# Performance work log

Measured on AMD Instinct MI355X. Metric: run time of the kernel, lower is better.

Reference implementation:

```python
import jax, jax.numpy as jnp
import numpy as np

B, C, T, H, W = 32, 384, 16, 14, 14
K, NUM_SAMPLES, SIGMA = 8, 1000, 0.05
C2 = 2 * C  # ScoreNet doubles embed_dim internally


def setup_inputs() -> dict:
    key = jax.random.key(0)
    ks = jax.random.split(key, 12)
    def rn(k, shape, s=0.02):
        return jax.random.normal(k, shape, dtype=jnp.float32) * s
    return {
        "frames": jax.random.normal(ks[0], (B, C, T, H, W), dtype=jnp.float32),
        "noise": jax.random.normal(ks[1], (B, NUM_SAMPLES, T), dtype=jnp.float32),
        "conv_w": rn(ks[2], (C, C, 1, 3, 3)),
        "conv_b": jnp.zeros((C,), jnp.float32),
        "bn_g": jnp.ones((C,), jnp.float32),
        "bn_b": jnp.zeros((C,), jnp.float32),
        "ln_g": jnp.ones((C2,), jnp.float32),
        "ln_b": jnp.zeros((C2,), jnp.float32),
        "lin_w": rn(ks[3], (C2, C2)),
        "lin_b": jnp.zeros((C2,), jnp.float32),
        "w1": rn(ks[4], (C2, C)), "b1": jnp.zeros((C,), jnp.float32),
        "w2": rn(ks[5], (C, C // 2)), "b2": jnp.zeros((C // 2,), jnp.float32),
        "w3": rn(ks[6], (C // 2, 1)), "b3": jnp.zeros((1,), jnp.float32),
    }


def score_net(frames, conv_w, conv_b, bn_g, bn_b, ln_g, ln_b, lin_w, lin_b,
              w1, b1, w2, b2, w3, b3):
    x = jax.lax.stop_gradient(frames)  # ScoreNet detaches its input
    x = jax.lax.conv_general_dilated(
        x, conv_w, window_strides=(1, 2, 2), padding='VALID',
        dimension_numbers=('NCDHW', 'OIDHW', 'NCDHW'))
    x = x + conv_b[None, :, None, None, None]
    # BatchNorm3d in training mode: biased batch stats over (N,T,H,W)
    m = x.mean(axis=(0, 2, 3, 4))
    v = x.var(axis=(0, 2, 3, 4))
    x = (x - m[None, :, None, None, None]) / jnp.sqrt(v + 1e-5)[None, :, None, None, None]
    x = x * bn_g[None, :, None, None, None] + bn_b[None, :, None, None, None]
    # b c t h w -> b t (h w) c
    b, c, t, h, w = x.shape
    x = jnp.transpose(x, (0, 2, 3, 4, 1)).reshape(b, t, h * w, c)
    x = jnp.concatenate([x.mean(axis=2), x.max(axis=2)], axis=-1)  # [B,T,2C]
    # LayerNorm(2C)
    mu = x.mean(-1, keepdims=True)
    var = x.var(-1, keepdims=True)
    x = (x - mu) / jnp.sqrt(var + 1e-5) * ln_g + ln_b
    x = jax.nn.gelu(x @ lin_w + lin_b, approximate=False)
    local_x = x[..., :C2 // 2]
    global_x = jnp.broadcast_to(x[..., C2 // 2:].mean(axis=1, keepdims=True), (b, t, C2 // 2))
    x = jnp.concatenate([local_x, global_x], axis=-1)
    x = jax.nn.gelu(x @ w1 + b1, approximate=False)
    x = jax.nn.gelu(x @ w2 + b2, approximate=False)
    score = (x @ w3 + b3)[..., 0]  # [B,T]
    smin = score.min(axis=-1, keepdims=True)
    smax = score.max(axis=-1, keepdims=True)
    return (score - smin) / (smax - smin + 1e-5)


def perturbed_indicators(score, noise):
    d = score.shape[-1]
    pert = score[:, None, :] + noise * SIGMA  # [B,N,T]
    idx_top = jnp.sort(jax.lax.top_k(pert, K)[1], axis=-1)        # [B,N,K]
    idx_back = jnp.sort(jax.lax.top_k(-pert, d - K)[1], axis=-1)  # [B,N,T-K]
    ind_top = jax.nn.one_hot(idx_top, d, dtype=jnp.float32).mean(axis=1)   # [B,K,T]
    ind_back = jax.nn.one_hot(idx_back, d, dtype=jnp.float32).mean(axis=1)  # [B,T-K,T]
    return ind_top, ind_back


def reference(frames, noise, conv_w, conv_b, bn_g, bn_b, ln_g, ln_b, lin_w, lin_b,
              w1, b1, w2, b2, w3, b3):
    score = score_net(frames, conv_w, conv_b, bn_g, bn_b, ln_g, ln_b, lin_w, lin_b,
                      w1, b1, w2, b2, w3, b3)  # [B,T]
    ind_top, ind_back = perturbed_indicators(score, noise)
    # b c t h w -> b t (h w c)
    flat = jnp.transpose(frames, (0, 2, 3, 4, 1)).reshape(B, T, H * W * C)
    p_top = jnp.einsum('bkd,bdc->bkc', ind_top, flat)
    p_back = jnp.einsum('bkd,bdc->bkc', ind_back, flat)
    frames_topk = jnp.transpose(p_top.reshape(B, K, H, W, C), (0, 4, 1, 2, 3))
    frames_back = jnp.transpose(p_back.reshape(B, T - K, H, W, C), (0, 4, 1, 2, 3))
    sorted_inds = jnp.argsort(score, axis=1)
    return frames_topk, frames_back, sorted_inds
```

## Files before the change

kernel.cpp:

```cpp
#include <hip/hip_runtime.h>
#include <hip/hip_bf16.h>
#include <cstdint>

#define NB 32
#define NC 384
#define NT 16
#define NH 14
#define NW 14
#define HWI 196
#define HOW 6
#define HWO 36
#define C2 768
#define MCONV (NB*NT*HWO)
#define KCONV 3456
#define TOPK 8
#define NSAMP 1000
#define OUT_TOPK_ELEMS (NB*NC*TOPK*HWI)
#define OUT_INDS_OFF   (2*OUT_TOPK_ELEMS)

#define OFF_FHI  0ull
#define OFF_FLO  77070336ull
#define OFF_WHI  154140672ull
#define OFF_WLO  156794880ull
#define OFF_CONV 159449088ull
#define OFF_PART 0ull
#define OFF_BNSC 221184ull
#define OFF_BNSH 222720ull
#define OFF_Y    224256ull
#define OFF_X1   1797120ull
#define OFF_GM   3369984ull
#define OFF_X2   3419136ull
#define OFF_H1   4992000ull
#define OFF_H2   5778432ull
#define OFF_IND  6171648ull

typedef __attribute__((ext_vector_type(4))) float f32x4;
typedef __attribute__((ext_vector_type(8))) short bf16x8;

__device__ __forceinline__ unsigned short f2bf(float f) {
  unsigned u = __float_as_uint(f);
  unsigned r = (u + 0x7FFFu + ((u >> 16) & 1u)) >> 16;
  return (unsigned short)r;
}
__device__ __forceinline__ float bf2f(unsigned short u) {
  return __uint_as_float(((unsigned)u) << 16);
}

__device__ __forceinline__ void gload_lds16(const void* gptr, void* lptr) {
  __builtin_amdgcn_global_load_lds(
      (const __attribute__((address_space(1))) unsigned int*)gptr,
      (__attribute__((address_space(3))) unsigned int*)lptr, 16, 0, 0);
}

__global__ __launch_bounds__(256)
void split_frames(const float* __restrict__ fr,
                  unsigned short* __restrict__ fhi,
                  unsigned short* __restrict__ flo) {
  __shared__ float tile[64][50];
  int bid = blockIdx.x;
  int cb = bid % 6;
  int r  = bid / 6;
  int hwb = r % 4;
  int bt  = r / 4;
  int c0 = cb * 64, hw0 = hwb * 49;
  int b = bt >> 4, t = bt & 15;
  size_t base = (((size_t)b * NC + c0) * NT + t) * HWI + hw0;
  for (int idx = threadIdx.x; idx < 64 * 49; idx += 256) {
    int c = idx / 49, hw = idx % 49;
    tile[c][hw] = fr[base + (size_t)c * (NT * HWI) + hw];
  }
  __syncthreads();
  size_t obase = ((size_t)bt * HWI + hw0) * NC + c0;
  for (int idx = threadIdx.x; idx < 64 * 49; idx += 256) {
    int hw = idx >> 6, c = idx & 63;
    float v = tile[c][hw];
    unsigned short h = f2bf(v);
    unsigned short l = f2bf(v - bf2f(h));
    size_t o = obase + (size_t)hw * NC + c;
    fhi[o] = h; flo[o] = l;
  }
}

__global__ __launch_bounds__(256)
void split_w(const float* __restrict__ cw,
             unsigned short* __restrict__ whi,
             unsigned short* __restrict__ wlo) {
  int idx = blockIdx.x * 256 + threadIdx.x;
  int co = idx / KCONV;
  int rem = idx - co * KCONV;
  int c9 = rem / NC, ci = rem - c9 * NC;
  float v = cw[((size_t)co * NC + ci) * 9 + c9];
  unsigned short h = f2bf(v);
  unsigned short l = f2bf(v - bf2f(h));
  whi[idx] = h; wlo[idx] = l;
}

__global__ __launch_bounds__(256, 2)
void conv_gemm(const unsigned short* __restrict__ fhi,
               const unsigned short* __restrict__ flo,
               const unsigned short* __restrict__ whi,
               const unsigned short* __restrict__ wlo,
               const float* __restrict__ conv_b,
               float* __restrict__ out) {
  __shared__ unsigned short sAhi[128 * 32], sAlo[128 * 32];
  __shared__ unsigned short sBhi[128 * 32], sBlo[128 * 32];
  const int tid = threadIdx.x;
  const int lane = tid & 63;
  const int wv = tid >> 6;
  const int bid = blockIdx.x;
  const int bm = bid % 144;
  const int bn = bid / 144;

  int aoff[2], boff[2];
#pragma unroll
  for (int j = 0; j < 2; ++j) {
    int l = (wv * 2 + j) * 64 + lane;
    int row = l >> 2, chunk = l & 3;
    int m = bm * 128 + row;
    int wo = m % 6; int tmp = m / 6;
    int ho = tmp % 6; tmp /= 6;
    aoff[j] = ((tmp * HWI) + (2 * ho) * NW + 2 * wo) * NC + chunk * 8;
    int co = bn * 128 + row;
    boff[j] = co * KCONV + chunk * 8;
  }

  f32x4 acc[4][4];
#pragma unroll
  for (int i = 0; i < 4; ++i)
#pragma unroll
    for (int j = 0; j < 4; ++j) acc[i][j] = (f32x4){0.f, 0.f, 0.f, 0.f};

  const int wrow = (wv >> 1) * 64;
  const int wcol = (wv & 1) * 64;
  const int fr_row = lane & 15;
  const int fr_k = (lane >> 4) * 8;

  for (int step = 0; step < 108; ++step) {
    int c9 = step / 12;
    int cis = (step - c9 * 12) * 32;
    int kh = c9 / 3, kw = c9 - kh * 3;
    int soffA = (kh * NW + kw) * NC + cis;
    int soffB = c9 * NC + cis;
#pragma unroll
    for (int j = 0; j < 2; ++j) {
      char* ldsA = (char*)sAhi + (wv * 2 + j) * 1024;
      char* ldsAl = (char*)sAlo + (wv * 2 + j) * 1024;
      char* ldsB = (char*)sBhi + (wv * 2 + j) * 1024;
      char* ldsBl = (char*)sBlo + (wv * 2 + j) * 1024;
      gload_lds16(fhi + aoff[j] + soffA, ldsA);
      gload_lds16(flo + aoff[j] + soffA, ldsAl);
      gload_lds16(whi + boff[j] + soffB, ldsB);
      gload_lds16(wlo + boff[j] + soffB, ldsBl);
    }
    __syncthreads();
    bf16x8 ah[4], al[4], bh[4], bl[4];
#pragma unroll
    for (int m = 0; m < 4; ++m) {
      int r = wrow + m * 16 + fr_row;
      ah[m] = *(const bf16x8*)&sAhi[r * 32 + fr_k];
      al[m] = *(const bf16x8*)&sAlo[r * 32 + fr_k];
    }
#pragma unroll
    for (int n = 0; n < 4; ++n) {
      int r = wcol + n * 16 + fr_row;
      bh[n] = *(const bf16x8*)&sBhi[r * 32 + fr_k];
      bl[n] = *(const bf16x8*)&sBlo[r * 32 + fr_k];
    }
#pragma unroll
    for (int m = 0; m < 4; ++m)
#pragma unroll
      for (int n = 0; n < 4; ++n) {
        acc[m][n] = __builtin_amdgcn_mfma_f32_16x16x32_bf16(ah[m], bh[n], acc[m][n], 0, 0, 0);
        acc[m][n] = __builtin_amdgcn_mfma_f32_16x16x32_bf16(ah[m], bl[n], acc[m][n], 0, 0, 0);
        acc[m][n] = __builtin_amdgcn_mfma_f32_16x16x32_bf16(al[m], bh[n], acc[m][n], 0, 0, 0);
      }
    __syncthreads();
  }

#pragma unroll
  for (int m = 0; m < 4; ++m)
#pragma unroll
    for (int n = 0; n < 4; ++n) {
      int col = bn * 128 + wcol + n * 16 + (lane & 15);
      float cb = conv_b[col];
#pragma unroll
      for (int j = 0; j < 4; ++j) {
        int row = bm * 128 + wrow + m * 16 + (lane >> 4) * 4 + j;
        out[(size_t)row * NC + col] = acc[m][n][j] + cb;
      }
    }
}

__global__ __launch_bounds__(384)
void bn_part(const float* __restrict__ conv, float* __restrict__ part) {
  int c = threadIdx.x;
  int r0 = blockIdx.x * 256;
  float s = 0.f, sq = 0.f;
  for (int r = 0; r < 256; ++r) {
    float v = conv[(size_t)(r0 + r) * NC + c];
    s += v; sq += v * v;
  }
  part[blockIdx.x * 768 + c] = s;
  part[blockIdx.x * 768 + 384 + c] = sq;
}

__global__ __launch_bounds__(384)
void bn_fin(const float* __restrict__ part, const float* __restrict__ bn_g,
            const float* __restrict__ bn_b, float* __restrict__ bnsc,
            float* __restrict__ bnsh) {
  int c = threadIdx.x;
  float s = 0.f, sq = 0.f;
  for (int i = 0; i < 72; ++i) {
    s += part[i * 768 + c];
    sq += part[i * 768 + 384 + c];
  }
  float mean = s / (float)MCONV;
  float var = sq / (float)MCONV - mean * mean;
  float sc = bn_g[c] / sqrtf(var + 1e-5f);
  bnsc[c] = sc;
  bnsh[c] = bn_b[c] - mean * sc;
}

__global__ __launch_bounds__(384)
void pool_ln(const float* __restrict__ conv, const float* __restrict__ bnsc,
             const float* __restrict__ bnsh, const float* __restrict__ ln_g,
             const float* __restrict__ ln_b, float* __restrict__ y) {
  __shared__ float r1[384], r2[384], stats[2];
  int bt = blockIdx.x, c = threadIdx.x;
  float sc = bnsc[c], sh = bnsh[c];
  const float* p = conv + (size_t)bt * HWO * NC + c;
  float sum = 0.f, mx = -1e30f;
  for (int hw = 0; hw < HWO; ++hw) {
    float v = p[hw * NC] * sc + sh;
    sum += v;
    mx = fmaxf(mx, v);
  }
  float meanv = sum * (1.f / 36.f);
  r1[c] = meanv + mx;
  r2[c] = meanv * meanv + mx * mx;
  __syncthreads();
  for (int s = 192; s >= 6; s >>= 1) {
    if (c < s) { r1[c] += r1[c + s]; r2[c] += r2[c + s]; }
    __syncthreads();
  }
  if (c == 0) {
    float S1 = 0.f, S2 = 0.f;
    for (int i = 0; i < 6; ++i) { S1 += r1[i]; S2 += r2[i]; }
    float mu = S1 / (float)C2;
    float var = S2 / (float)C2 - mu * mu;
    stats[0] = mu;
    stats[1] = 1.0f / sqrtf(var + 1e-5f);
  }
  __syncthreads();
  float mu = stats[0], rstd = stats[1];
  y[(size_t)bt * C2 + c] = (meanv - mu) * rstd * ln_g[c] + ln_b[c];
  y[(size_t)bt * C2 + 384 + c] = (mx - mu) * rstd * ln_g[384 + c] + ln_b[384 + c];
}

template <int GELU>
__global__ __launch_bounds__(256)
void gemm64(const float* __restrict__ A, const float* __restrict__ Wm,
            const float* __restrict__ bias, float* __restrict__ Cm,
            int K, int N) {
  __shared__ float As[64][17];
  __shared__ float Bs[16][68];
  int tid = threadIdx.x;
  int tx = tid & 15, ty = tid >> 4;
  int m0 = blockIdx.y * 64, n0 = blockIdx.x * 64;
  int ar = tid >> 2, ak = (tid & 3) * 4;
  int br = tid >> 4, bc = (tid & 15) * 4;
  float acc[4][4] = {};
  for (int kt = 0; kt < K; kt += 16) {
    float4 av = *(const float4*)(A + (size_t)(m0 + ar) * K + kt + ak);
    float4 bv = *(const float4*)(Wm + (size_t)(kt + br) * N + n0 + bc);
    As[ar][ak + 0] = av.x; As[ar][ak + 1] = av.y;
    As[ar][ak + 2] = av.z; As[ar][ak + 3] = av.w;
    Bs[br][bc + 0] = bv.x; Bs[br][bc + 1] = bv.y;
    Bs[br][bc + 2] = bv.z; Bs[br][bc + 3] = bv.w;
    __syncthreads();
#pragma unroll
    for (int kk = 0; kk < 16; ++kk) {
      float a0 = As[ty * 4 + 0][kk], a1 = As[ty * 4 + 1][kk];
      float a2 = As[ty * 4 + 2][kk], a3 = As[ty * 4 + 3][kk];
      float b0 = Bs[kk][tx * 4 + 0], b1 = Bs[kk][tx * 4 + 1];
      float b2 = Bs[kk][tx * 4 + 2], b3 = Bs[kk][tx * 4 + 3];
      acc[0][0] += a0 * b0; acc[0][1] += a0 * b1; acc[0][2] += a0 * b2; acc[0][3] += a0 * b3;
      acc[1][0] += a1 * b0; acc[1][1] += a1 * b1; acc[1][2] += a1 * b2; acc[1][3] += a1 * b3;
      acc[2][0] += a2 * b0; acc[2][1] += a2 * b1; acc[2][2] += a2 * b2; acc[2][3] += a2 * b3;
      acc[3][0] += a3 * b0; acc[3][1] += a3 * b1; acc[3][2] += a3 * b2; acc[3][3] += a3 * b3;
    }
    __syncthreads();
  }
#pragma unroll
  for (int i = 0; i < 4; ++i) {
    int row = m0 + ty * 4 + i;
#pragma unroll
    for (int j = 0; j < 4; ++j) {
      int col = n0 + tx * 4 + j;
      float v = acc[i][j] + bias[col];
      if (GELU) v = 0.5f * v * (1.0f + erff(v * 0.70710678118654752f));
      Cm[(size_t)row * N + col] = v;
    }
  }
}

__global__ __launch_bounds__(384)
void gmean_k(const float* __restrict__ x1, float* __restrict__ gm) {
  int b = blockIdx.x, c = threadIdx.x;
  float s = 0.f;
  for (int t = 0; t < NT; ++t) s += x1[((size_t)b * NT + t) * C2 + 384 + c];
  gm[b * 384 + c] = s * (1.f / 16.f);
}

__global__ __launch_bounds__(256)
void buildx2(const float* __restrict__ x1, const float* __restrict__ gm,
             float* __restrict__ x2) {
  int idx = blockIdx.x * 256 + threadIdx.x;
  int bt = idx / C2, c = idx - bt * C2;
  float v = (c < 384) ? x1[(size_t)bt * C2 + c] : gm[(bt >> 4) * 384 + (c - 384)];
  x2[idx] = v;
}

__global__ __launch_bounds__(256)
void score_head(const float* __restrict__ h2, const float* __restrict__ w3,
                const float* __restrict__ b3, const float* __restrict__ noise,
                float* __restrict__ ind, float* __restrict__ out_inds) {
  int b = blockIdx.x;
  int tid = threadIdx.x;
  int lane = tid & 63, wv = tid >> 6;
  __shared__ float sv[16], sn[16];
  __shared__ unsigned cnt[256];
  for (int t = wv; t < 16; t += 4) {
    const float* hr = h2 + ((size_t)b * 16 + t) * 192;
    float p = 0.f;
    for (int i = lane; i < 192; i += 64) p += hr[i] * w3[i];
#pragma unroll
    for (int off = 32; off; off >>= 1) p += __shfl_down(p, off, 64);
    if (lane == 0) sv[t] = p + b3[0];
  }
  cnt[tid] = 0;
  __syncthreads();
  if (tid == 0) {
    float mn = sv[0], mx = sv[0];
    for (int t = 1; t < 16; ++t) { mn = fminf(mn, sv[t]); mx = fmaxf(mx, sv[t]); }
    float inv = 1.0f / (mx - mn + 1e-5f);
    for (int t = 0; t < 16; ++t) sn[t] = (sv[t] - mn) * inv;
  }
  __syncthreads();
  if (tid < 16) {
    int t = tid, r = 0;
    for (int u = 0; u < 16; ++u)
      r += (sv[u] < sv[t]) || (sv[u] == sv[t] && u < t);
    out_inds[b * 16 + r] = (float)t;
  }
  for (int s = tid; s < NSAMP; s += 256) {
    const float* nz = noise + ((size_t)b * NSAMP + s) * 16;
    float pert[16];
#pragma unroll
    for (int t = 0; t < 16; ++t) pert[t] = sn[t] + 0.05f * nz[t];
    unsigned tm = 0, bm2 = 0;
#pragma unroll
    for (int t = 0; t < 16; ++t) {
      int ct = 0, cb = 0;
#pragma unroll
      for (int u = 0; u < 16; ++u) {
        ct += (pert[u] > pert[t]) || (pert[u] == pert[t] && u < t);
        cb += (pert[u] < pert[t]) || (pert[u] == pert[t] && u < t);
      }
      if (ct < 8) tm |= 1u << t;
      if (cb < 8) bm2 |= 1u << t;
    }
    int j = 0, jb = 0;
#pragma unroll
    for (int t = 0; t < 16; ++t) {
      if (tm & (1u << t)) { if (j < 8) atomicAdd(&cnt[j * 16 + t], 1u); ++j; }
      if (bm2 & (1u << t)) { if (jb < 8) atomicAdd(&cnt[128 + jb * 16 + t], 1u); ++jb; }
    }
  }
  __syncthreads();
  ind[b * 256 + tid] = (float)cnt[tid] / 1000.0f;
}

__global__ __launch_bounds__(256)
void gather_k(const float* __restrict__ frames, const float* __restrict__ ind,
              float* __restrict__ out) {
  int bc = blockIdx.x;
  int b = bc / NC;
  __shared__ float wt[256];
  wt[threadIdx.x] = ind[b * 256 + threadIdx.x];
  __syncthreads();
  int hw = threadIdx.x;
  if (hw >= HWI) return;
  const float* src = frames + (size_t)bc * NT * HWI + hw;
  float v[16];
#pragma unroll
  for (int t = 0; t < 16; ++t) v[t] = src[t * HWI];
  size_t obase = (size_t)bc * TOPK * HWI + hw;
#pragma unroll
  for (int k = 0; k < TOPK; ++k) {
    float st = 0.f, sb = 0.f;
#pragma unroll
    for (int t = 0; t < 16; ++t) {
      st += wt[k * 16 + t] * v[t];
      sb += wt[128 + k * 16 + t] * v[t];
    }
    out[obase + k * HWI] = st;
    out[OUT_TOPK_ELEMS + obase + k * HWI] = sb;
  }
}

extern "C" void kernel_launch(void* const* d_in, const int* in_sizes, int n_in,
                              void* d_out, int out_size, void* d_ws, size_t ws_size,
                              hipStream_t stream) {
  const float* frames = (const float*)d_in[0];
  const float* noise  = (const float*)d_in[1];
  const float* conv_w = (const float*)d_in[2];
  const float* conv_b = (const float*)d_in[3];
  const float* bn_g   = (const float*)d_in[4];
  const float* bn_b   = (const float*)d_in[5];
  const float* ln_g   = (const float*)d_in[6];
  const float* ln_b   = (const float*)d_in[7];
  const float* lin_w  = (const float*)d_in[8];
  const float* lin_b  = (const float*)d_in[9];
  const float* w1     = (const float*)d_in[10];
  const float* b1     = (const float*)d_in[11];
  const float* w2     = (const float*)d_in[12];
  const float* b2     = (const float*)d_in[13];
  const float* w3     = (const float*)d_in[14];
  const float* b3     = (const float*)d_in[15];

  char* ws = (char*)d_ws;
  unsigned short* fhi = (unsigned short*)(ws + OFF_FHI);
  unsigned short* flo = (unsigned short*)(ws + OFF_FLO);
  unsigned short* whi = (unsigned short*)(ws + OFF_WHI);
  unsigned short* wlo = (unsigned short*)(ws + OFF_WLO);
  float* convo = (float*)(ws + OFF_CONV);
  float* part  = (float*)(ws + OFF_PART);
  float* bnsc  = (float*)(ws + OFF_BNSC);
  float* bnsh  = (float*)(ws + OFF_BNSH);
  float* y     = (float*)(ws + OFF_Y);
  float* x1    = (float*)(ws + OFF_X1);
  float* gm    = (float*)(ws + OFF_GM);
  float* x2    = (float*)(ws + OFF_X2);
  float* h1    = (float*)(ws + OFF_H1);
  float* h2    = (float*)(ws + OFF_H2);
  float* ind   = (float*)(ws + OFF_IND);
  float* out   = (float*)d_out;

  split_frames<<<12288, 256, 0, stream>>>(frames, fhi, flo);
  split_w<<<5184, 256, 0, stream>>>(conv_w, whi, wlo);
  conv_gemm<<<432, 256, 0, stream>>>(fhi, flo, whi, wlo, conv_b, convo);
  bn_part<<<72, 384, 0, stream>>>(convo, part);
  bn_fin<<<1, 384, 0, stream>>>(part, bn_g, bn_b, bnsc, bnsh);
  pool_ln<<<512, 384, 0, stream>>>(convo, bnsc, bnsh, ln_g, ln_b, y);
  gemm64<1><<<dim3(12, 8), 256, 0, stream>>>(y, lin_w, lin_b, x1, 768, 768);
  gmean_k<<<32, 384, 0, stream>>>(x1, gm);
  buildx2<<<1536, 256, 0, stream>>>(x1, gm, x2);
  gemm64<1><<<dim3(6, 8), 256, 0, stream>>>(x2, w1, b1, h1, 768, 384);
  gemm64<1><<<dim3(3, 8), 256, 0, stream>>>(h1, w2, b2, h2, 384, 192);
  score_head<<<32, 256, 0, stream>>>(h2, w3, b3, noise, ind, out + OUT_INDS_OFF);
  gather_k<<<12288, 256, 0, stream>>>(frames, ind, out);
}
```

Before: 520.5 us.

## Split conv GEMM over K, vectorize frame split, fuse x2 build into GEMM

The conv GEMM is split into two K halves across twice as many blocks. Each half writes its own partial output, and the output buffer serves as scratch for the second half. The BN statistics and pooling kernels sum the two partials. split_frames now processes whole (b,t) slices with float4 loads and packed bf16x8 stores, and the buildx2 kernel is removed by reading the global mean directly inside the GEMM load. The aim is better CU occupancy for the 432-block conv and less memory traffic, at the cost of an extra partial buffer's write and read.

```diff
diff --git a/kernel.cpp b/kernel.cpp
--- a/kernel.cpp
+++ b/kernel.cpp
@@ -29,7 +29,6 @@
 #define OFF_Y    224256ull
 #define OFF_X1   1797120ull
 #define OFF_GM   3369984ull
-#define OFF_X2   3419136ull
 #define OFF_H1   4992000ull
 #define OFF_H2   5778432ull
 #define OFF_IND  6171648ull
@@ -56,28 +55,36 @@
 void split_frames(const float* __restrict__ fr,
                   unsigned short* __restrict__ fhi,
                   unsigned short* __restrict__ flo) {
-  __shared__ float tile[64][50];
+  __shared__ unsigned int tile[64][197];
   int bid = blockIdx.x;
-  int cb = bid % 6;
-  int r  = bid / 6;
-  int hwb = r % 4;
-  int bt  = r / 4;
-  int c0 = cb * 64, hw0 = hwb * 49;
+  int cb = bid % 6, bt = bid / 6;
   int b = bt >> 4, t = bt & 15;
-  size_t base = (((size_t)b * NC + c0) * NT + t) * HWI + hw0;
-  for (int idx = threadIdx.x; idx < 64 * 49; idx += 256) {
-    int c = idx / 49, hw = idx % 49;
-    tile[c][hw] = fr[base + (size_t)c * (NT * HWI) + hw];
-  }
-  __syncthreads();
-  size_t obase = ((size_t)bt * HWI + hw0) * NC + c0;
-  for (int idx = threadIdx.x; idx < 64 * 49; idx += 256) {
-    int hw = idx >> 6, c = idx & 63;
-    float v = tile[c][hw];
-    unsigned short h = f2bf(v);
-    unsigned short l = f2bf(v - bf2f(h));
-    size_t o = obase + (size_t)hw * NC + c;
-    fhi[o] = h; flo[o] = l;
+  const float* src = fr + (((size_t)b * NC + cb * 64) * NT + t) * HWI;
+  for (int i = threadIdx.x; i < 64 * 49; i += 256) {
+    int c = i / 49, q = i - c * 49;
+    float4 v = *(const float4*)(src + (size_t)c * (NT * HWI) + q * 4);
+    float vv[4] = {v.x, v.y, v.z, v.w};
+#pragma unroll
+    for (int u = 0; u < 4; ++u) {
+      unsigned short h = f2bf(vv[u]);
+      unsigned short l = f2bf(vv[u] - bf2f(h));
+      tile[c][q * 4 + u] = ((unsigned)h << 16) | (unsigned)l;
+    }
+  }
+  __syncthreads();
+  size_t obase = ((size_t)bt * HWI) * NC + cb * 64;
+  for (int i = threadIdx.x; i < 196 * 8; i += 256) {
+    int hw = i >> 3, c8 = i & 7;
+    bf16x8 vh, vl;
+#pragma unroll
+    for (int u = 0; u < 8; ++u) {
+      unsigned p = tile[c8 * 8 + u][hw];
+      vh[u] = (short)(p >> 16);
+      vl[u] = (short)(p & 0xffff);
+    }
+    size_t o = obase + (size_t)hw * NC + c8 * 8;
+    *(bf16x8*)(fhi + o) = vh;
+    *(bf16x8*)(flo + o) = vl;
   }
 }
 
@@ -101,7 +108,8 @@
                const unsigned short* __restrict__ whi,
                const unsigned short* __restrict__ wlo,
                const float* __restrict__ conv_b,
-               float* __restrict__ out) {
+               float* __restrict__ p0,
+               float* __restrict__ p1) {
   __shared__ unsigned short sAhi[128 * 32], sAlo[128 * 32];
   __shared__ unsigned short sBhi[128 * 32], sBlo[128 * 32];
   const int tid = threadIdx.x;
@@ -109,7 +117,9 @@
   const int wv = tid >> 6;
   const int bid = blockIdx.x;
   const int bm = bid % 144;
-  const int bn = bid / 144;
+  const int r  = bid / 144;
+  const int bn = r % 3;
+  const int kz = r / 3;
 
   int aoff[2], boff[2];
 #pragma unroll
@@ -135,17 +145,17 @@
   const int fr_row = lane & 15;
   const int fr_k = (lane >> 4) * 8;
 
-  for (int step = 0; step < 108; ++step) {
-    int c9 = step / 12;
-    int cis = (step - c9 * 12) * 32;
+  int c9 = kz ? 4 : 0;
+  int rem = kz ? 6 : 0;
+  for (int s = 0; s < 54; ++s) {
     int kh = c9 / 3, kw = c9 - kh * 3;
-    int soffA = (kh * NW + kw) * NC + cis;
-    int soffB = c9 * NC + cis;
+    int soffA = (kh * NW + kw) * NC + rem * 32;
+    int soffB = c9 * NC + rem * 32;
 #pragma unroll
     for (int j = 0; j < 2; ++j) {
-      char* ldsA = (char*)sAhi + (wv * 2 + j) * 1024;
+      char* ldsA  = (char*)sAhi + (wv * 2 + j) * 1024;
       char* ldsAl = (char*)sAlo + (wv * 2 + j) * 1024;
-      char* ldsB = (char*)sBhi + (wv * 2 + j) * 1024;
+      char* ldsB  = (char*)sBhi + (wv * 2 + j) * 1024;
       char* ldsBl = (char*)sBlo + (wv * 2 + j) * 1024;
       gload_lds16(fhi + aoff[j] + soffA, ldsA);
       gload_lds16(flo + aoff[j] + soffA, ldsAl);
@@ -156,15 +166,15 @@
     bf16x8 ah[4], al[4], bh[4], bl[4];
 #pragma unroll
     for (int m = 0; m < 4; ++m) {
-      int r = wrow + m * 16 + fr_row;
-      ah[m] = *(const bf16x8*)&sAhi[r * 32 + fr_k];
-      al[m] = *(const bf16x8*)&sAlo[r * 32 + fr_k];
+      int rr = wrow + m * 16 + fr_row;
+      ah[m] = *(const bf16x8*)&sAhi[rr * 32 + fr_k];
+      al[m] = *(const bf16x8*)&sAlo[rr * 32 + fr_k];
     }
 #pragma unroll
     for (int n = 0; n < 4; ++n) {
-      int r = wcol + n * 16 + fr_row;
-      bh[n] = *(const bf16x8*)&sBhi[r * 32 + fr_k];
-      bl[n] = *(const bf16x8*)&sBlo[r * 32 + fr_k];
+      int rr = wcol + n * 16 + fr_row;
+      bh[n] = *(const bf16x8*)&sBhi[rr * 32 + fr_k];
+      bl[n] = *(const bf16x8*)&sBlo[rr * 32 + fr_k];
     }
 #pragma unroll
     for (int m = 0; m < 4; ++m)
@@ -175,29 +185,33 @@
         acc[m][n] = __builtin_amdgcn_mfma_f32_16x16x32_bf16(al[m], bh[n], acc[m][n], 0, 0, 0);
       }
     __syncthreads();
-  }
-
+    if (++rem == 12) { rem = 0; ++c9; }
+  }
+
+  float* dst = kz ? p1 : p0;
 #pragma unroll
   for (int m = 0; m < 4; ++m)
 #pragma unroll
     for (int n = 0; n < 4; ++n) {
       int col = bn * 128 + wcol + n * 16 + (lane & 15);
-      float cb = conv_b[col];
+      float cb = kz ? 0.f : conv_b[col];
 #pragma unroll
       for (int j = 0; j < 4; ++j) {
         int row = bm * 128 + wrow + m * 16 + (lane >> 4) * 4 + j;
-        out[(size_t)row * NC + col] = acc[m][n][j] + cb;
+        dst[(size_t)row * NC + col] = acc[m][n][j] + cb;
       }
     }
 }
 
 __global__ __launch_bounds__(384)
-void bn_part(const float* __restrict__ conv, float* __restrict__ part) {
+void bn_part(const float* __restrict__ p0, const float* __restrict__ p1,
+             float* __restrict__ part) {
   int c = threadIdx.x;
   int r0 = blockIdx.x * 256;
   float s = 0.f, sq = 0.f;
   for (int r = 0; r < 256; ++r) {
-    float v = conv[(size_t)(r0 + r) * NC + c];
+    size_t off = (size_t)(r0 + r) * NC + c;
+    float v = p0[off] + p1[off];
     s += v; sq += v * v;
   }
   part[blockIdx.x * 768 + c] = s;
@@ -222,16 +236,18 @@
 }
 
 __global__ __launch_bounds__(384)
-void pool_ln(const float* __restrict__ conv, const float* __restrict__ bnsc,
+void pool_ln(const float* __restrict__ p0, const float* __restrict__ p1,
+             const float* __restrict__ bnsc,
              const float* __restrict__ bnsh, const float* __restrict__ ln_g,
              const float* __restrict__ ln_b, float* __restrict__ y) {
   __shared__ float r1[384], r2[384], stats[2];
   int bt = blockIdx.x, c = threadIdx.x;
   float sc = bnsc[c], sh = bnsh[c];
-  const float* p = conv + (size_t)bt * HWO * NC + c;
+  size_t base = (size_t)bt * HWO * NC + c;
   float sum = 0.f, mx = -1e30f;
   for (int hw = 0; hw < HWO; ++hw) {
-    float v = p[hw * NC] * sc + sh;
+    size_t off = base + (size_t)hw * NC;
+    float v = (p0[off] + p1[off]) * sc + sh;
     sum += v;
     mx = fmaxf(mx, v);
   }
@@ -257,9 +273,10 @@
   y[(size_t)bt * C2 + 384 + c] = (mx - mu) * rstd * ln_g[384 + c] + ln_b[384 + c];
 }
 
-template <int GELU>
+template <int GELU, int X2>
 __global__ __launch_bounds__(256)
-void gemm64(const float* __restrict__ A, const float* __restrict__ Wm,
+void gemm64(const float* __restrict__ A, const float* __restrict__ gmv,
+            const float* __restrict__ Wm,
             const float* __restrict__ bias, float* __restrict__ Cm,
             int K, int N) {
   __shared__ float As[64][17];
@@ -271,7 +288,12 @@
   int br = tid >> 4, bc = (tid & 15) * 4;
   float acc[4][4] = {};
   for (int kt = 0; kt < K; kt += 16) {
-    float4 av = *(const float4*)(A + (size_t)(m0 + ar) * K + kt + ak);
+    int kcol = kt + ak;
+    float4 av;
+    if (X2 && kcol >= 384)
+      av = *(const float4*)(gmv + ((m0 + ar) >> 4) * 384 + (kcol - 384));
+    else
+      av = *(const float4*)(A + (size_t)(m0 + ar) * K + kcol);
     float4 bv = *(const float4*)(Wm + (size_t)(kt + br) * N + n0 + bc);
     As[ar][ak + 0] = av.x; As[ar][ak + 1] = av.y;
     As[ar][ak + 2] = av.z; As[ar][ak + 3] = av.w;
@@ -310,15 +332,6 @@
   float s = 0.f;
   for (int t = 0; t < NT; ++t) s += x1[((size_t)b * NT + t) * C2 + 384 + c];
   gm[b * 384 + c] = s * (1.f / 16.f);
-}
-
-__global__ __launch_bounds__(256)
-void buildx2(const float* __restrict__ x1, const float* __restrict__ gm,
-             float* __restrict__ x2) {
-  int idx = blockIdx.x * 256 + threadIdx.x;
-  int bt = idx / C2, c = idx - bt * C2;
-  float v = (c < 384) ? x1[(size_t)bt * C2 + c] : gm[(bt >> 4) * 384 + (c - 384)];
-  x2[idx] = v;
 }
 
 __global__ __launch_bounds__(256)
@@ -434,30 +447,29 @@
   unsigned short* flo = (unsigned short*)(ws + OFF_FLO);
   unsigned short* whi = (unsigned short*)(ws + OFF_WHI);
   unsigned short* wlo = (unsigned short*)(ws + OFF_WLO);
-  float* convo = (float*)(ws + OFF_CONV);
+  float* p0    = (float*)(ws + OFF_CONV);
   float* part  = (float*)(ws + OFF_PART);
   float* bnsc  = (float*)(ws + OFF_BNSC);
   float* bnsh  = (float*)(ws + OFF_BNSH);
   float* y     = (float*)(ws + OFF_Y);
   float* x1    = (float*)(ws + OFF_X1);
   float* gm    = (float*)(ws + OFF_GM);
-  float* x2    = (float*)(ws + OFF_X2);
   float* h1    = (float*)(ws + OFF_H1);
   float* h2    = (float*)(ws + OFF_H2);
   float* ind   = (float*)(ws + OFF_IND);
   float* out   = (float*)d_out;
-
-  split_frames<<<12288, 256, 0, stream>>>(frames, fhi, flo);
+  float* p1    = out;
+
+  split_frames<<<3072, 256, 0, stream>>>(frames, fhi, flo);
   split_w<<<5184, 256, 0, stream>>>(conv_w, whi, wlo);
-  conv_gemm<<<432, 256, 0, stream>>>(fhi, flo, whi, wlo, conv_b, convo);
-  bn_part<<<72, 384, 0, stream>>>(convo, part);
+  conv_gemm<<<864, 256, 0, stream>>>(fhi, flo, whi, wlo, conv_b, p0, p1);
+  bn_part<<<72, 384, 0, stream>>>(p0, p1, part);
   bn_fin<<<1, 384, 0, stream>>>(part, bn_g, bn_b, bnsc, bnsh);
-  pool_ln<<<512, 384, 0, stream>>>(convo, bnsc, bnsh, ln_g, ln_b, y);
-  gemm64<1><<<dim3(12, 8), 256, 0, stream>>>(y, lin_w, lin_b, x1, 768, 768);
+  pool_ln<<<512, 384, 0, stream>>>(p0, p1, bnsc, bnsh, ln_g, ln_b, y);
+  gemm64<1, 0><<<dim3(12, 8), 256, 0, stream>>>(y, nullptr, lin_w, lin_b, x1, 768, 768);
   gmean_k<<<32, 384, 0, stream>>>(x1, gm);
-  buildx2<<<1536, 256, 0, stream>>>(x1, gm, x2);
-  gemm64<1><<<dim3(6, 8), 256, 0, stream>>>(x2, w1, b1, h1, 768, 384);
-  gemm64<1><<<dim3(3, 8), 256, 0, stream>>>(h1, w2, b2, h2, 384, 192);
+  gemm64<1, 1><<<dim3(6, 8), 256, 0, stream>>>(x1, gm, w1, b1, h1, 768, 384);
+  gemm64<1, 0><<<dim3(3, 8), 256, 0, stream>>>(h1, nullptr, w2, b2, h2, 384, 192);
   score_head<<<32, 256, 0, stream>>>(h2, w3, b3, noise, ind, out + OUT_INDS_OFF);
   gather_k<<<12288, 256, 0, stream>>>(frames, ind, out);
 }
```

New measurement: 520.7 us. Within noise of the previous version (+0.1%).
